# Kernel tuning notes

Hardware: AMD Instinct MI355X
Metric: run time of the kernel (lower is better)

## Reference

```python
import jax, jax.numpy as jnp
import numpy as np

N = 50000   # team_count (num nodes)
E = 800000  # num edges
D = 64      # embed_dim
C = 32      # conv_out_channels
K = 3       # Chebyshev order
B = 16384   # number of games (len(home))


def setup_inputs() -> dict:
    key = jax.random.key(0)
    ks = jax.random.split(key, 20)
    inp = {
        "edge_index": jax.random.randint(ks[0], (2, E), 0, N),
        "home": jax.random.randint(ks[1], (B,), 0, N),
        "away": jax.random.randint(ks[2], (B,), 0, N),
        "edge_weight": jax.random.uniform(ks[3], (E,), dtype=jnp.float32),
        "embedding": jax.random.normal(ks[4], (N, D), dtype=jnp.float32) * 0.1,
    }
    def W(k, i, o):
        return jax.random.normal(k, (K, i, o), dtype=jnp.float32) * 0.05
    inp["Wxz"] = W(ks[5], D, C); inp["Whz"] = W(ks[6], C, C)
    inp["Wxr"] = W(ks[7], D, C); inp["Whr"] = W(ks[8], C, C)
    inp["Wxh"] = W(ks[9], D, C); inp["Whh"] = W(ks[10], C, C)
    for i, name in enumerate(["bxz", "bhz", "bxr", "bhr", "bxh", "bhh"]):
        inp[name] = jax.random.normal(ks[11 + i], (C,), dtype=jnp.float32) * 0.01
    return inp


def _cheb(x, W, b, row, col, w_hat, n):
    """PyG ChebConv with sym normalization, lambda_max=2: L_hat = -D^-1/2 A D^-1/2."""
    def prop(t):  # L_hat @ t  via gather->scale->scatter over edges
        return jax.ops.segment_sum(w_hat[:, None] * t[row], col, num_segments=n)
    Tx0 = x
    out = Tx0 @ W[0]
    Tx1 = prop(Tx0)
    out = out + Tx1 @ W[1]
    for k in range(2, W.shape[0]):
        Tx2 = 2.0 * prop(Tx1) - Tx0
        out = out + Tx2 @ W[k]
        Tx0, Tx1 = Tx1, Tx2
    return out + b


def reference(edge_index, home, away, edge_weight, embedding,
              Wxz, Whz, Wxr, Whr, Wxh, Whh,
              bxz, bhz, bxr, bhr, bxh, bhh):
    row, col = edge_index[0], edge_index[1]
    n = embedding.shape[0]
    deg = jax.ops.segment_sum(edge_weight, row, num_segments=n)
    dinv = jnp.where(deg > 0, jax.lax.rsqrt(deg), 0.0)
    w_hat = -dinv[row] * edge_weight * dinv[col]

    x = embedding                       # [N, D]
    H = jnp.zeros((n, Wxz.shape[-1]), x.dtype)  # initial hidden state
    cheb = lambda t, W, b: _cheb(t, W, b, row, col, w_hat, n)

    Z = jax.nn.sigmoid(cheb(x, Wxz, bxz) + cheb(H, Whz, bhz))
    R = jax.nn.sigmoid(cheb(x, Wxr, bxr) + cheb(H, Whr, bhr))
    H_tilde = jnp.tanh(cheb(x, Wxh, bxh) + cheb(H * R, Whh, bhh))
    H = Z * H + (1.0 - Z) * H_tilde     # [N, C]

    h = jnp.concatenate([H[home], H[away]], axis=0)  # [2B, C]
    return jax.nn.softmax(h, axis=0)    # torch Softmax(dim=0)
```

## Files before the change

### kernel.cpp

```cpp
#include <hip/hip_runtime.h>
#include <hip/hip_fp16.h>
#include <math.h>

constexpr int N_   = 50000;
constexpr int E_   = 800000;
constexpr int D_   = 64;
constexpr int C_   = 32;
constexpr int B_   = 16384;
constexpr int TWOB = 2 * B_;
constexpr int NB_SM = 256;
constexpr int NBINS = (N_ + 255) / 256;
constexpr int EPB   = 4096;
constexpr int NCH   = (E_ + EPB - 1) / EPB;
constexpr int CAPBB = 64;
constexpr int CAPB  = 5120;
constexpr int GN  = 64;
constexpr int LDP = 68;
constexpr int NPAD = 50176;

__device__ inline float4 ld_h4(const ushort* p) {
    uint2 u = *reinterpret_cast<const uint2*>(p);
    __half2 h0 = *reinterpret_cast<__half2*>(&u.x);
    __half2 h1 = *reinterpret_cast<__half2*>(&u.y);
    float2 f0 = __half22float2(h0), f1 = __half22float2(h1);
    return make_float4(f0.x, f0.y, f1.x, f1.y);
}
__device__ inline void st_h4(ushort* p, float4 v) {
    __half2 h0 = __floats2half2_rn(v.x, v.y);
    __half2 h1 = __floats2half2_rn(v.z, v.w);
    uint2 u;
    u.x = *reinterpret_cast<unsigned*>(&h0);
    u.y = *reinterpret_cast<unsigned*>(&h1);
    *reinterpret_cast<uint2*>(p) = u;
}

__device__ inline void excl_scan256(int* sc, int t, int c0, int* st) {
    sc[t] = c0;
    __syncthreads();
#pragma unroll
    for (int off = 1; off < 256; off <<= 1) {
        int v = (t >= off) ? sc[t - off] : 0;
        __syncthreads();
        sc[t] += v;
        __syncthreads();
    }
    st[t] = sc[t] - c0;
}

__global__ __launch_bounds__(256) void k_bin(const int* __restrict__ row,
                                             const int* __restrict__ col,
                                             const float* __restrict__ ew,
                                             int* __restrict__ colCnt,
                                             int* __restrict__ rowCnt,
                                             int2* __restrict__ colBins2,
                                             int2* __restrict__ rowBins2) {
    __shared__ int cnt[256], st[256], cur[256], sc[256];
    __shared__ int2 buf[EPB];
    int t = threadIdx.x, blk = blockIdx.x;
    int base = blk * EPB;
    int nE = min(EPB, E_ - base);

    cnt[t] = 0;
    __syncthreads();
    for (int i = t; i < nE; i += 256) atomicAdd(&cnt[col[base + i] >> 8], 1);
    __syncthreads();
    int c0 = cnt[t];
    excl_scan256(sc, t, c0, st);
    cur[t] = 0;
    __syncthreads();
    for (int i = t; i < nE; i += 256) {
        int c = col[base + i], r = row[base + i];
        float w = ew[base + i];
        int p = st[c >> 8] + atomicAdd(&cur[c >> 8], 1);
        buf[p] = make_int2((c << 16) | r, __float_as_int(w));
    }
    __syncthreads();
    for (int i = t; i < nE; i += 256) {
        int2 e = buf[i];
        int bin = (int)(((unsigned)e.x) >> 24);
        int local = i - st[bin];
        if (local < CAPBB) colBins2[((size_t)bin * NCH + blk) * CAPBB + local] = e;
    }
    colCnt[blk * 256 + t] = min(c0, CAPBB);
    __syncthreads();

    cnt[t] = 0;
    __syncthreads();
    for (int i = t; i < nE; i += 256) atomicAdd(&cnt[row[base + i] >> 8], 1);
    __syncthreads();
    c0 = cnt[t];
    excl_scan256(sc, t, c0, st);
    cur[t] = 0;
    __syncthreads();
    for (int i = t; i < nE; i += 256) {
        int r = row[base + i];
        float w = ew[base + i];
        int p = st[r >> 8] + atomicAdd(&cur[r >> 8], 1);
        buf[p] = make_int2(r, __float_as_int(w));
    }
    __syncthreads();
    for (int i = t; i < nE; i += 256) {
        int2 e = buf[i];
        int bin = (int)(((unsigned)e.x) >> 8);
        int local = i - st[bin];
        if (local < CAPBB) rowBins2[((size_t)bin * NCH + blk) * CAPBB + local] = e;
    }
    rowCnt[blk * 256 + t] = min(c0, CAPBB);
}

__global__ __launch_bounds__(256) void k_deg(const int* __restrict__ rowCnt,
                                             const int2* __restrict__ rowBins2,
                                             float* __restrict__ dinv) {
    __shared__ float acc[256];
    int t = threadIdx.x, b = blockIdx.x;
    acc[t] = 0.f;
    __syncthreads();
    if (t < NCH) {
        int n = rowCnt[t * 256 + b];
        const int2* ch = rowBins2 + ((size_t)b * NCH + t) * CAPBB;
        for (int i = 0; i < n; ++i) {
            int2 e = ch[i];
            atomicAdd(&acc[e.x & 255], __int_as_float(e.y));
        }
    }
    __syncthreads();
    int r = b * 256 + t;
    if (r < N_) {
        float d = acc[t];
        dinv[r] = (d > 0.f) ? 1.f / sqrtf(d) : 0.f;
    }
}

__global__ __launch_bounds__(256) void k_sort(const int* __restrict__ colCnt,
                                              const int2* __restrict__ colBins2,
                                              const float* __restrict__ dinv,
                                              int2* __restrict__ edges,
                                              int2* __restrict__ percol,
                                              float* __restrict__ colsum) {
    __shared__ int cnt[256], st[256], cur[256], sc[256], pref[256];
    __shared__ int2 sbuf[CAPB];
    int t = threadIdx.x, b = blockIdx.x;
    if (b == 0 && t < 64) colsum[t] = 0.f;
    int myc = (t < NCH) ? colCnt[t * 256 + b] : 0;
    excl_scan256(sc, t, myc, pref);
    cnt[t] = 0;
    __syncthreads();
    if (t < NCH) {
        const int2* ch = colBins2 + ((size_t)b * NCH + t) * CAPBB;
        int p0 = pref[t];
        for (int i = 0; i < myc; ++i) {
            if (p0 + i < CAPB) {
                int2 e = ch[i];
                sbuf[p0 + i] = e;
                atomicAdd(&cnt[(((unsigned)e.x) >> 16) & 255], 1);
            }
        }
    }
    __syncthreads();
    int nb = min(sc[255], CAPB);
    int c0 = cnt[t];
    __syncthreads();
    excl_scan256(sc, t, c0, st);
    cur[t] = 0;
    __syncthreads();
    for (int i = t; i < nb; i += 256) {
        int2 e = sbuf[i];
        unsigned m = (unsigned)e.x;
        int r = (int)(m & 0xffffu);
        int c = (int)(m >> 16);
        float w = -__int_as_float(e.y) * dinv[r] * dinv[c];
        int clow = c & 255;
        int p = st[clow] + atomicAdd(&cur[clow], 1);
        edges[b * CAPB + p] = make_int2(r, __float_as_int(w));
    }
    percol[b * 256 + t] = make_int2(b * CAPB + st[t], cnt[t]);
}

__global__ __launch_bounds__(256) void k_prop1(const int2* __restrict__ percol,
                                               const int2* __restrict__ edges,
                                               const float* __restrict__ x,
                                               ushort* __restrict__ tx1h) {
    int node = (blockIdx.x * 256 + threadIdx.x) >> 6;
    if (node >= N_) return;
    int lane = threadIdx.x & 63;
    int eslot = lane >> 4;
    int f4 = (lane & 15) << 2;
    int2 oc = percol[node];
    int beg = oc.x, n = oc.y;
    float4 acc = {0.f, 0.f, 0.f, 0.f};
    for (int cb = 0; cb < n; cb += 16) {
        int2 er = edges[beg + cb + (lane & 15)];
        int   rr = er.x;
        float wr = __int_as_float(er.y);
#pragma unroll
        for (int k = 0; k < 4; ++k) {
            int idx = cb + 4 * k + eslot;
            int   r = __shfl(rr, 4 * k + eslot, 64);
            float w = __shfl(wr, 4 * k + eslot, 64);
            bool ok = idx < n;
            int  rs = ok ? r : 0;
            float wm = ok ? w : 0.f;
            float4 v = *reinterpret_cast<const float4*>(x + (size_t)rs * D_ + f4);
            acc.x += wm * v.x;
            acc.y += wm * v.y;
            acc.z += wm * v.z;
            acc.w += wm * v.w;
        }
    }
    acc.x += __shfl_xor(acc.x, 16, 64); acc.y += __shfl_xor(acc.y, 16, 64);
    acc.z += __shfl_xor(acc.z, 16, 64); acc.w += __shfl_xor(acc.w, 16, 64);
    acc.x += __shfl_xor(acc.x, 32, 64); acc.y += __shfl_xor(acc.y, 32, 64);
    acc.z += __shfl_xor(acc.z, 32, 64); acc.w += __shfl_xor(acc.w, 32, 64);
    if (eslot == 0) st_h4(tx1h + (size_t)node * D_ + f4, acc);
}

__global__ __launch_bounds__(256) void k_pg(const int2* __restrict__ percol,
                                            const int2* __restrict__ edges,
                                            const ushort* __restrict__ tx1h,
                                            const float* __restrict__ x,
                                            const float* __restrict__ Wxz,
                                            const float* __restrict__ Wxh,
                                            const float* __restrict__ bxz,
                                            const float* __restrict__ bhz,
                                            const float* __restrict__ bxh,
                                            const float* __restrict__ bhh,
                                            float* __restrict__ H) {
    __shared__ float lA[GN * LDP];
    __shared__ float lB[D_ * LDP];
    int t = threadIdx.x;
    int node0 = blockIdx.x * GN;
    int valid = min(GN, N_ - node0);
    int w = t >> 6, lane = t & 63, eslot = lane >> 4, f4 = (lane & 15) << 2;

    for (int j = 0; j < 16; ++j) {
        int nl = w * 16 + j;
        int node = node0 + nl;
        if (node < N_) {
            int2 oc = percol[node];
            int beg = oc.x, n = oc.y;
            float4 acc = {0.f, 0.f, 0.f, 0.f};
            for (int cb = 0; cb < n; cb += 16) {
                int2 er = edges[beg + cb + (lane & 15)];
                int   rr = er.x;
                float wr = __int_as_float(er.y);
#pragma unroll
                for (int k = 0; k < 4; ++k) {
                    int idx = cb + 4 * k + eslot;
                    int   r = __shfl(rr, 4 * k + eslot, 64);
                    float ww = __shfl(wr, 4 * k + eslot, 64);
                    bool ok = idx < n;
                    int  rs = ok ? r : 0;
                    float wm = ok ? ww : 0.f;
                    float4 v = ld_h4(tx1h + (size_t)rs * D_ + f4);
                    acc.x += wm * v.x;
                    acc.y += wm * v.y;
                    acc.z += wm * v.z;
                    acc.w += wm * v.w;
                }
            }
            acc.x += __shfl_xor(acc.x, 16, 64); acc.y += __shfl_xor(acc.y, 16, 64);
            acc.z += __shfl_xor(acc.z, 16, 64); acc.w += __shfl_xor(acc.w, 16, 64);
            acc.x += __shfl_xor(acc.x, 32, 64); acc.y += __shfl_xor(acc.y, 32, 64);
            acc.z += __shfl_xor(acc.z, 32, 64); acc.w += __shfl_xor(acc.w, 32, 64);
            if (eslot == 0) {
                float4 xv = *reinterpret_cast<const float4*>(x + (size_t)node * D_ + f4);
                float4 o = {2.f * acc.x - xv.x, 2.f * acc.y - xv.y,
                            2.f * acc.z - xv.z, 2.f * acc.w - xv.w};
                *reinterpret_cast<float4*>(&lA[nl * LDP + f4]) = o;
            }
        } else if (eslot == 0) {
            float4 z = {0.f, 0.f, 0.f, 0.f};
            *reinterpret_cast<float4*>(&lA[nl * LDP + f4]) = z;
        }
    }
    __syncthreads();

    int tn = t >> 4, tc = t & 15;
    float acc2[4][4] = {};
    for (int cc = 0; cc < 3; ++cc) {
        int ch = (cc == 0) ? 2 : (cc == 1) ? 0 : 1;
        if (cc) {
            if (ch == 0) {
                const float* s = x + (size_t)node0 * D_;
#pragma unroll
                for (int j = 0; j < 4; ++j) {
                    int q = t * 4 + j * 1024;
                    int nd = q >> 6, dd = q & 63;
                    float4 v = {0.f, 0.f, 0.f, 0.f};
                    if (nd < valid) v = *reinterpret_cast<const float4*>(s + q);
                    *reinterpret_cast<float4*>(&lA[nd * LDP + dd]) = v;
                }
            } else {
                const ushort* s = tx1h + (size_t)node0 * D_;
#pragma unroll
                for (int j = 0; j < 4; ++j) {
                    int q = t * 4 + j * 1024;
                    int nd = q >> 6, dd = q & 63;
                    float4 v = {0.f, 0.f, 0.f, 0.f};
                    if (nd < valid) v = ld_h4(s + q);
                    *reinterpret_cast<float4*>(&lA[nd * LDP + dd]) = v;
                }
            }
        }
#pragma unroll
        for (int j = 0; j < 4; ++j) {
            int q = t * 4 + j * 1024;
            int dd = q >> 6, jj = q & 63;
            const float* wsrc = (jj < 32) ? (Wxz + ch * 2048 + dd * 32 + jj)
                                          : (Wxh + ch * 2048 + dd * 32 + (jj - 32));
            *reinterpret_cast<float4*>(&lB[dd * LDP + jj]) =
                *reinterpret_cast<const float4*>(wsrc);
        }
        __syncthreads();
#pragma unroll 4
        for (int k0 = 0; k0 < D_; k0 += 4) {
            float4 a[4], b[4];
#pragma unroll
            for (int i = 0; i < 4; ++i)
                a[i] = *reinterpret_cast<const float4*>(&lA[(tn * 4 + i) * LDP + k0]);
#pragma unroll
            for (int kk = 0; kk < 4; ++kk)
                b[kk] = *reinterpret_cast<const float4*>(&lB[(k0 + kk) * LDP + tc * 4]);
#pragma unroll
            for (int i = 0; i < 4; ++i) {
                acc2[i][0] += a[i].x * b[0].x + a[i].y * b[1].x + a[i].z * b[2].x + a[i].w * b[3].x;
                acc2[i][1] += a[i].x * b[0].y + a[i].y * b[1].y + a[i].z * b[2].y + a[i].w * b[3].y;
                acc2[i][2] += a[i].x * b[0].z + a[i].y * b[1].z + a[i].z * b[2].z + a[i].w * b[3].z;
                acc2[i][3] += a[i].x * b[0].w + a[i].y * b[1].w + a[i].z * b[2].w + a[i].w * b[3].w;
            }
        }
        __syncthreads();
    }
#pragma unroll
    for (int i = 0; i < 4; ++i) {
        float4 v = {acc2[i][0], acc2[i][1], acc2[i][2], acc2[i][3]};
        *reinterpret_cast<float4*>(&lA[(tn * 4 + i) * LDP + tc * 4]) = v;
    }
    __syncthreads();
#pragma unroll
    for (int m = 0; m < 8; ++m) {
        int idx = t + m * 256;
        int nd = idx >> 5, c = idx & 31;
        if (nd < valid) {
            float az = lA[nd * LDP + c]       + bxz[c] + bhz[c];
            float ah = lA[nd * LDP + 32 + c]  + bxh[c] + bhh[c];
            float z  = 1.f / (1.f + expf(-az));
            H[(size_t)(node0 + nd) * C_ + c] = (1.f - z) * tanhf(ah);
        }
    }
}

__global__ __launch_bounds__(256) void k_gexpsum2(const int* __restrict__ home,
                                                  const int* __restrict__ away,
                                                  const float* __restrict__ H,
                                                  float* __restrict__ hbuf,
                                                  float* __restrict__ colsum) {
    __shared__ float sm[8][32];
    int c = threadIdx.x & 31, g = threadIdx.x >> 5;
    float s = 0.f;
    for (int r0 = blockIdx.x * 8; r0 < TWOB; r0 += gridDim.x * 8) {
        int r = r0 + g;
        int node = (r < B_) ? home[r] : away[r - B_];
        float e = expf(H[(size_t)node * C_ + c]);
        hbuf[(size_t)r * C_ + c] = e;
        s += e;
    }
    sm[g][c] = s;
    __syncthreads();
    if (g < 4) sm[g][c] += sm[g + 4][c];
    __syncthreads();
    if (g < 2) sm[g][c] += sm[g + 2][c];
    __syncthreads();
    if (g == 0) atomicAdd(&colsum[c], sm[0][c] + sm[1][c]);
}

__global__ __launch_bounds__(256) void k_norm(const float* __restrict__ hbuf,
                                              const float* __restrict__ colsum,
                                              float* __restrict__ out) {
    int i = blockIdx.x * 256 + threadIdx.x;
    if (i < TWOB * C_ / 4) {
        float4 v = reinterpret_cast<const float4*>(hbuf)[i];
        int c0 = (i * 4) & 31;
        float4 s = *reinterpret_cast<const float4*>(colsum + c0);
        float4 o;
        o.x = v.x / s.x;
        o.y = v.y / s.y;
        o.z = v.z / s.z;
        o.w = v.w / s.w;
        reinterpret_cast<float4*>(out)[i] = o;
    }
}

extern "C" void kernel_launch(void* const* d_in, const int* in_sizes, int n_in,
                              void* d_out, int out_size, void* d_ws, size_t ws_size,
                              hipStream_t stream) {
    const int*   edge_index = (const int*)d_in[0];
    const int*   row  = edge_index;
    const int*   col  = edge_index + E_;
    const int*   home = (const int*)d_in[1];
    const int*   away = (const int*)d_in[2];
    const float* ew   = (const float*)d_in[3];
    const float* x    = (const float*)d_in[4];
    const float* Wxz  = (const float*)d_in[5];
    const float* Wxh  = (const float*)d_in[9];
    const float* bxz  = (const float*)d_in[11];
    const float* bhz  = (const float*)d_in[12];
    const float* bxh  = (const float*)d_in[15];
    const float* bhh  = (const float*)d_in[16];
    float* out = (float*)d_out;
    float* ws = (float*)d_ws;

    const size_t o_colCnt  = 0;
    const size_t o_rowCnt  = o_colCnt + (size_t)NCH * 256;
    const size_t o_colsum  = o_rowCnt + (size_t)NCH * 256;
    const size_t o_dinv    = o_colsum + 64;
    const size_t o_colBins2 = o_dinv + NPAD;
    const size_t o_rowBins2 = o_colBins2 + 2 * (size_t)NBINS * NCH * CAPBB;
    const size_t o_edges   = o_rowBins2 + 2 * (size_t)NBINS * NCH * CAPBB;
    const size_t o_percol  = o_edges + 2 * (size_t)NBINS * CAPB + 32;
    const size_t o_tx1h    = o_percol + 2 * (size_t)NBINS * 256;
    const size_t o_H       = o_rowBins2;
    const size_t o_hbuf    = o_colBins2;

    int*    colCnt   = (int*)(ws + o_colCnt);
    int*    rowCnt   = (int*)(ws + o_rowCnt);
    int2*   colBins2 = (int2*)(ws + o_colBins2);
    int2*   rowBins2 = (int2*)(ws + o_rowBins2);
    int2*   edges    = (int2*)(ws + o_edges);
    int2*   percol   = (int2*)(ws + o_percol);
    ushort* tx1h     = (ushort*)(ws + o_tx1h);

    k_bin <<<NCH, 256, 0, stream>>>(row, col, ew, colCnt, rowCnt, colBins2, rowBins2);
    k_deg <<<NBINS, 256, 0, stream>>>(rowCnt, rowBins2, ws + o_dinv);
    k_sort<<<NBINS, 256, 0, stream>>>(colCnt, colBins2, ws + o_dinv, edges, percol, ws + o_colsum);

    k_prop1<<<(N_ * 64 + 255) / 256, 256, 0, stream>>>(percol, edges, x, tx1h);

    k_pg<<<(N_ + GN - 1) / GN, 256, 0, stream>>>(percol, edges, tx1h, x,
                                                 Wxz, Wxh, bxz, bhz, bxh, bhh, ws + o_H);

    k_gexpsum2<<<NB_SM, 256, 0, stream>>>(home, away, ws + o_H, ws + o_hbuf, ws + o_colsum);
    k_norm    <<<(TWOB * C_ / 4 + 255) / 256, 256, 0, stream>>>(ws + o_hbuf, ws + o_colsum, out);
}
```

Baseline: 155.8 us.

## Split fused second propagation and gate GEMM into separate prop2 and gates kernels

The previous kernel did the second sparse propagation for 64 nodes per block and then ran the gate GEMM on the same data. That put 16 serial node gathers per wave ahead of a shared-memory GEMM. The new code moves the gather into its own kernel with one wave per node, writing Tx2 as fp16 to a new workspace buffer, and a separate kernel that does the three-chunk GEMM and gate activations. This raises parallelism and latency hiding for the gather. The cost is an extra launch, an extra fp16 round trip through global memory for Tx2, and one more rounding of Tx2 to half precision.

```diff
diff --git a/kernel.cpp b/kernel.cpp
--- a/kernel.cpp
+++ b/kernel.cpp
@@ -214,92 +214,87 @@
     if (eslot == 0) st_h4(tx1h + (size_t)node * D_ + f4, acc);
 }
 
-__global__ __launch_bounds__(256) void k_pg(const int2* __restrict__ percol,
-                                            const int2* __restrict__ edges,
-                                            const ushort* __restrict__ tx1h,
-                                            const float* __restrict__ x,
-                                            const float* __restrict__ Wxz,
-                                            const float* __restrict__ Wxh,
-                                            const float* __restrict__ bxz,
-                                            const float* __restrict__ bhz,
-                                            const float* __restrict__ bxh,
-                                            const float* __restrict__ bhh,
-                                            float* __restrict__ H) {
+__global__ __launch_bounds__(256) void k_prop2(const int2* __restrict__ percol,
+                                               const int2* __restrict__ edges,
+                                               const ushort* __restrict__ tx1h,
+                                               const float* __restrict__ x,
+                                               ushort* __restrict__ tx2h) {
+    int node = (blockIdx.x * 256 + threadIdx.x) >> 6;
+    if (node >= N_) return;
+    int lane = threadIdx.x & 63;
+    int eslot = lane >> 4;
+    int f4 = (lane & 15) << 2;
+    int2 oc = percol[node];
+    int beg = oc.x, n = oc.y;
+    float4 acc = {0.f, 0.f, 0.f, 0.f};
+    for (int cb = 0; cb < n; cb += 16) {
+        int2 er = edges[beg + cb + (lane & 15)];
+        int   rr = er.x;
+        float wr = __int_as_float(er.y);
+#pragma unroll
+        for (int k = 0; k < 4; ++k) {
+            int idx = cb + 4 * k + eslot;
+            int   r = __shfl(rr, 4 * k + eslot, 64);
+            float w = __shfl(wr, 4 * k + eslot, 64);
+            bool ok = idx < n;
+            int  rs = ok ? r : 0;
+            float wm = ok ? w : 0.f;
+            float4 v = ld_h4(tx1h + (size_t)rs * D_ + f4);
+            acc.x += wm * v.x;
+            acc.y += wm * v.y;
+            acc.z += wm * v.z;
+            acc.w += wm * v.w;
+        }
+    }
+    acc.x += __shfl_xor(acc.x, 16, 64); acc.y += __shfl_xor(acc.y, 16, 64);
+    acc.z += __shfl_xor(acc.z, 16, 64); acc.w += __shfl_xor(acc.w, 16, 64);
+    acc.x += __shfl_xor(acc.x, 32, 64); acc.y += __shfl_xor(acc.y, 32, 64);
+    acc.z += __shfl_xor(acc.z, 32, 64); acc.w += __shfl_xor(acc.w, 32, 64);
+    if (eslot == 0) {
+        float4 xv = *reinterpret_cast<const float4*>(x + (size_t)node * D_ + f4);
+        float4 o = {2.f * acc.x - xv.x, 2.f * acc.y - xv.y,
+                    2.f * acc.z - xv.z, 2.f * acc.w - xv.w};
+        st_h4(tx2h + (size_t)node * D_ + f4, o);
+    }
+}
+
+__global__ __launch_bounds__(256) void k_gates(const float* __restrict__ x,
+                                               const ushort* __restrict__ tx1h,
+                                               const ushort* __restrict__ tx2h,
+                                               const float* __restrict__ Wxz,
+                                               const float* __restrict__ Wxh,
+                                               const float* __restrict__ bxz,
+                                               const float* __restrict__ bhz,
+                                               const float* __restrict__ bxh,
+                                               const float* __restrict__ bhh,
+                                               float* __restrict__ H) {
     __shared__ float lA[GN * LDP];
     __shared__ float lB[D_ * LDP];
     int t = threadIdx.x;
     int node0 = blockIdx.x * GN;
     int valid = min(GN, N_ - node0);
-    int w = t >> 6, lane = t & 63, eslot = lane >> 4, f4 = (lane & 15) << 2;
-
-    for (int j = 0; j < 16; ++j) {
-        int nl = w * 16 + j;
-        int node = node0 + nl;
-        if (node < N_) {
-            int2 oc = percol[node];
-            int beg = oc.x, n = oc.y;
-            float4 acc = {0.f, 0.f, 0.f, 0.f};
-            for (int cb = 0; cb < n; cb += 16) {
-                int2 er = edges[beg + cb + (lane & 15)];
-                int   rr = er.x;
-                float wr = __int_as_float(er.y);
-#pragma unroll
-                for (int k = 0; k < 4; ++k) {
-                    int idx = cb + 4 * k + eslot;
-                    int   r = __shfl(rr, 4 * k + eslot, 64);
-                    float ww = __shfl(wr, 4 * k + eslot, 64);
-                    bool ok = idx < n;
-                    int  rs = ok ? r : 0;
-                    float wm = ok ? ww : 0.f;
-                    float4 v = ld_h4(tx1h + (size_t)rs * D_ + f4);
-                    acc.x += wm * v.x;
-                    acc.y += wm * v.y;
-                    acc.z += wm * v.z;
-                    acc.w += wm * v.w;
-                }
+    int tn = t >> 4, tc = t & 15;
+    float acc[4][4] = {};
+    for (int ch = 0; ch < 3; ++ch) {
+        if (ch == 0) {
+            const float* s = x + (size_t)node0 * D_;
+#pragma unroll
+            for (int j = 0; j < 4; ++j) {
+                int q = t * 4 + j * 1024;
+                int nd = q >> 6, dd = q & 63;
+                float4 v = {0.f, 0.f, 0.f, 0.f};
+                if (nd < valid) v = *reinterpret_cast<const float4*>(s + q);
+                *reinterpret_cast<float4*>(&lA[nd * LDP + dd]) = v;
             }
-            acc.x += __shfl_xor(acc.x, 16, 64); acc.y += __shfl_xor(acc.y, 16, 64);
-            acc.z += __shfl_xor(acc.z, 16, 64); acc.w += __shfl_xor(acc.w, 16, 64);
-            acc.x += __shfl_xor(acc.x, 32, 64); acc.y += __shfl_xor(acc.y, 32, 64);
-            acc.z += __shfl_xor(acc.z, 32, 64); acc.w += __shfl_xor(acc.w, 32, 64);
-            if (eslot == 0) {
-                float4 xv = *reinterpret_cast<const float4*>(x + (size_t)node * D_ + f4);
-                float4 o = {2.f * acc.x - xv.x, 2.f * acc.y - xv.y,
-                            2.f * acc.z - xv.z, 2.f * acc.w - xv.w};
-                *reinterpret_cast<float4*>(&lA[nl * LDP + f4]) = o;
-            }
-        } else if (eslot == 0) {
-            float4 z = {0.f, 0.f, 0.f, 0.f};
-            *reinterpret_cast<float4*>(&lA[nl * LDP + f4]) = z;
-        }
-    }
-    __syncthreads();
-
-    int tn = t >> 4, tc = t & 15;
-    float acc2[4][4] = {};
-    for (int cc = 0; cc < 3; ++cc) {
-        int ch = (cc == 0) ? 2 : (cc == 1) ? 0 : 1;
-        if (cc) {
-            if (ch == 0) {
-                const float* s = x + (size_t)node0 * D_;
-#pragma unroll
-                for (int j = 0; j < 4; ++j) {
-                    int q = t * 4 + j * 1024;
-                    int nd = q >> 6, dd = q & 63;
-                    float4 v = {0.f, 0.f, 0.f, 0.f};
-                    if (nd < valid) v = *reinterpret_cast<const float4*>(s + q);
-                    *reinterpret_cast<float4*>(&lA[nd * LDP + dd]) = v;
-                }
-            } else {
-                const ushort* s = tx1h + (size_t)node0 * D_;
-#pragma unroll
-                for (int j = 0; j < 4; ++j) {
-                    int q = t * 4 + j * 1024;
-                    int nd = q >> 6, dd = q & 63;
-                    float4 v = {0.f, 0.f, 0.f, 0.f};
-                    if (nd < valid) v = ld_h4(s + q);
-                    *reinterpret_cast<float4*>(&lA[nd * LDP + dd]) = v;
-                }
+        } else {
+            const ushort* s = ((ch == 1) ? tx1h : tx2h) + (size_t)node0 * D_;
+#pragma unroll
+            for (int j = 0; j < 4; ++j) {
+                int q = t * 4 + j * 1024;
+                int nd = q >> 6, dd = q & 63;
+                float4 v = {0.f, 0.f, 0.f, 0.f};
+                if (nd < valid) v = ld_h4(s + q);
+                *reinterpret_cast<float4*>(&lA[nd * LDP + dd]) = v;
             }
         }
 #pragma unroll
@@ -323,17 +318,17 @@
                 b[kk] = *reinterpret_cast<const float4*>(&lB[(k0 + kk) * LDP + tc * 4]);
 #pragma unroll
             for (int i = 0; i < 4; ++i) {
-                acc2[i][0] += a[i].x * b[0].x + a[i].y * b[1].x + a[i].z * b[2].x + a[i].w * b[3].x;
-                acc2[i][1] += a[i].x * b[0].y + a[i].y * b[1].y + a[i].z * b[2].y + a[i].w * b[3].y;
-                acc2[i][2] += a[i].x * b[0].z + a[i].y * b[1].z + a[i].z * b[2].z + a[i].w * b[3].z;
-                acc2[i][3] += a[i].x * b[0].w + a[i].y * b[1].w + a[i].z * b[2].w + a[i].w * b[3].w;
+                acc[i][0] += a[i].x * b[0].x + a[i].y * b[1].x + a[i].z * b[2].x + a[i].w * b[3].x;
+                acc[i][1] += a[i].x * b[0].y + a[i].y * b[1].y + a[i].z * b[2].y + a[i].w * b[3].y;
+                acc[i][2] += a[i].x * b[0].z + a[i].y * b[1].z + a[i].z * b[2].z + a[i].w * b[3].z;
+                acc[i][3] += a[i].x * b[0].w + a[i].y * b[1].w + a[i].z * b[2].w + a[i].w * b[3].w;
             }
         }
         __syncthreads();
     }
 #pragma unroll
     for (int i = 0; i < 4; ++i) {
-        float4 v = {acc2[i][0], acc2[i][1], acc2[i][2], acc2[i][3]};
+        float4 v = {acc[i][0], acc[i][1], acc[i][2], acc[i][3]};
         *reinterpret_cast<float4*>(&lA[(tn * 4 + i) * LDP + tc * 4]) = v;
     }
     __syncthreads();
@@ -419,6 +414,7 @@
     const size_t o_edges   = o_rowBins2 + 2 * (size_t)NBINS * NCH * CAPBB;
     const size_t o_percol  = o_edges + 2 * (size_t)NBINS * CAPB + 32;
     const size_t o_tx1h    = o_percol + 2 * (size_t)NBINS * 256;
+    const size_t o_tx2h    = o_tx1h + (size_t)N_ * D_ / 2;
     const size_t o_H       = o_rowBins2;
     const size_t o_hbuf    = o_colBins2;
 
@@ -429,15 +425,17 @@
     int2*   edges    = (int2*)(ws + o_edges);
     int2*   percol   = (int2*)(ws + o_percol);
     ushort* tx1h     = (ushort*)(ws + o_tx1h);
+    ushort* tx2h     = (ushort*)(ws + o_tx2h);
 
     k_bin <<<NCH, 256, 0, stream>>>(row, col, ew, colCnt, rowCnt, colBins2, rowBins2);
     k_deg <<<NBINS, 256, 0, stream>>>(rowCnt, rowBins2, ws + o_dinv);
     k_sort<<<NBINS, 256, 0, stream>>>(colCnt, colBins2, ws + o_dinv, edges, percol, ws + o_colsum);
 
     k_prop1<<<(N_ * 64 + 255) / 256, 256, 0, stream>>>(percol, edges, x, tx1h);
-
-    k_pg<<<(N_ + GN - 1) / GN, 256, 0, stream>>>(percol, edges, tx1h, x,
-                                                 Wxz, Wxh, bxz, bhz, bxh, bhh, ws + o_H);
+    k_prop2<<<(N_ * 64 + 255) / 256, 256, 0, stream>>>(percol, edges, tx1h, x, tx2h);
+
+    k_gates<<<(N_ + GN - 1) / GN, 256, 0, stream>>>(x, tx1h, tx2h,
+                                                    Wxz, Wxh, bxz, bhz, bxh, bhh, ws + o_H);
 
     k_gexpsum2<<<NB_SM, 256, 0, stream>>>(home, away, ws + o_H, ws + o_hbuf, ws + o_colsum);
     k_norm    <<<(TWOB * C_ / 4 + 255) / 256, 256, 0, stream>>>(ws + o_hbuf, ws + o_colsum, out);
```

After: 145.4 us (median of 2 runs). -6.7%, faster.
